# Performance work log

Measured on AMD Instinct MI355X. Metric: run time of the kernel, lower is better.

The kernel has to match this reference:

```python
import jax, jax.numpy as jnp
import numpy as np

B, T, D, H, O = 64, 1000, 16, 1024, 8
DT, TAU, G, PROB_CONN = 0.1, 1.0, 1.5, 0.25


def setup_inputs() -> dict:
    key = jax.random.key(0)
    k_in, k_h0, k_i2h, k_mask, k_val, k_h2o = jax.random.split(key, 6)
    inp = jax.random.normal(k_in, (B, T, D), dtype=jnp.float32)
    hidden = jax.random.normal(k_h0, (B, H), dtype=jnp.float32)
    # i2h: 1/sqrt(D) * randn(H, D)
    W_i2h = jax.random.normal(k_i2h, (H, D), dtype=jnp.float32) / np.sqrt(D)
    # h2h: sparse Gaussian, connection prob PROB_CONN, no self-connections,
    # std = g / sqrt(prob_conn * H)
    mask = (jax.random.uniform(k_mask, (H, H)) < PROB_CONN).astype(jnp.float32)
    mask = mask * (1.0 - jnp.eye(H, dtype=jnp.float32))
    sigma = G / np.sqrt(PROB_CONN * H)
    W_h2h = jax.random.normal(k_val, (H, H), dtype=jnp.float32) * sigma * mask
    # h2o: 1/sqrt(H) * randn(O, H)
    W_h2o = jax.random.normal(k_h2o, (O, H), dtype=jnp.float32) / np.sqrt(H)
    return {"input": inp, "hidden": hidden, "W_i2h": W_i2h, "W_h2h": W_h2h, "W_h2o": W_h2o}


def reference(input, hidden, W_i2h, W_h2h, W_h2o):
    a = DT / TAU  # leak factor
    # precompute input projection for all timesteps: [B,T,H]
    x_proj = jnp.einsum('btd,hd->bth', input, W_i2h)
    xs = jnp.swapaxes(x_proj, 0, 1)  # [T,B,H]

    def step(h, x_t):
        h = (1.0 - a) * h + a * (jnp.tanh(h) @ W_h2h.T + x_t)
        out = jnp.tanh(h) @ W_h2o.T
        return h, (out, h)

    _, (outs, hs) = jax.lax.scan(step, hidden, xs)
    outputs = jnp.swapaxes(outs, 0, 1)  # [B,T,O]
    hiddens = jnp.swapaxes(hs, 0, 1)    # [B,T,H]
    return outputs, hiddens
```

## Files before the change

### kernel.cpp

```cpp
#include <hip/hip_runtime.h>
#include <hip/hip_bf16.h>

#define BB 64
#define TT 1000
#define DD 16
#define HH 1024
#define OO 8

#define NGRP 16
#define GB   4
#define SJ   64
#define NJS  16
#define NBLK 256
#define NTH  512

__global__ __launch_bounds__(NTH, 2) void rnn_coop(
    const float* __restrict__ x,
    const float* __restrict__ h0,
    const float* __restrict__ Wi2h,
    const float* Wh2h,
    float* __restrict__ out_h,
    float* TH,
    unsigned* flags)
{
    __shared__ __align__(16) float THl[8][4][GB][36];
    __shared__ float SC[2][GB][SJ][9];
    __shared__ float XS[2][GB][20];

    const int tid = threadIdx.x;
    const int w   = tid >> 6;
    const int l   = tid & 63;
    const int bid = blockIdx.x;
    const int bg  = bid & (NGRP - 1);
    const int js  = bid >> 4;

    const int j16 = l & 15;
    const int k4  = l >> 4;
    const int jbase = js * SJ + j16 * 4;
    const int kbase = w * 128 + k4 * 32;

    float4 w4[4][8];
#pragma unroll
    for (int jj = 0; jj < 4; ++jj)
#pragma unroll
        for (int kq = 0; kq < 8; ++kq)
            w4[jj][kq] = *(const float4*)&Wh2h[(size_t)(jbase + jj) * HH + kbase + kq * 4];
#pragma unroll
    for (int jj = 0; jj < 4; ++jj)
#pragma unroll
        for (int kq = 0; kq < 8; ++kq)
            asm volatile("" : "+v"(w4[jj][kq].x), "+v"(w4[jj][kq].y),
                             "+v"(w4[jj][kq].z), "+v"(w4[jj][kq].w));

    const int fb = tid >> 6, fj = tid & 63;
    float h = 0.f;
    float wi[DD];
    if (tid < 256) {
        h = h0[(size_t)(bg * GB + fb) * HH + js * SJ + fj];
#pragma unroll
        for (int d = 0; d < DD; ++d) wi[d] = Wi2h[(js * SJ + fj) * DD + d];
        float th0 = tanhf(h);
        __hip_atomic_store(&TH[((size_t)(0 * NGRP + bg) * GB + fb) * HH + js * SJ + fj],
                           th0, __ATOMIC_RELAXED, __HIP_MEMORY_SCOPE_AGENT);
        asm volatile("s_waitcnt vmcnt(0)" ::: "memory");
        if (l == 0)
            __hip_atomic_store(&flags[((size_t)(0 * NGRP + bg) * NJS + js) * 16 + fb],
                               1u, __ATOMIC_RELAXED, __HIP_MEMORY_SCOPE_AGENT);
    }

    for (int t = 0; t < TT; ++t) {
        const int p = t & 1;

        {
            const unsigned target = (unsigned)(t + 1);
            const unsigned* fa = flags +
                ((size_t)(p * NGRP + bg) * NJS + (2 * w + (l >> 2))) * 16 + (l & 3);
            for (;;) {
                unsigned v = target;
                if (l < 8)
                    v = __hip_atomic_load(fa, __ATOMIC_RELAXED, __HIP_MEMORY_SCOPE_AGENT);
                if (__all((int)(v >= target))) break;
                __builtin_amdgcn_s_sleep(1);
            }
        }

        {
            const int sb = l >> 4, sq = l & 15;
            const float* base = TH + ((size_t)(p * NGRP + bg) * GB + sb) * HH + w * 128;
            const float* a0 = base + sq * 4;
            const float* a1 = base + (sq + 16) * 4;
            float4 v0, v1;
            asm volatile("global_load_dwordx4 %0, %2, off sc0 sc1\n\t"
                         "global_load_dwordx4 %1, %3, off sc0 sc1\n\t"
                         "s_waitcnt vmcnt(0)"
                         : "=&v"(v0), "=&v"(v1)
                         : "v"(a0), "v"(a1)
                         : "memory");
            int k40 = sq >> 3,        kk0 = (sq & 7) ^ k40;
            int k41 = (sq + 16) >> 3, kk1 = (sq & 7) ^ k41;
            *(float4*)&THl[w][k40][sb][kk0 * 4] = v0;
            *(float4*)&THl[w][k41][sb][kk1 * 4] = v1;
        }
        if (w == 0) {
            int sb = l >> 2, dq = (l & 3) * 4;
            if (l < 16) {
                float4 v = *(const float4*)&x[((size_t)(bg * GB + sb) * TT + t) * DD + dq];
                *(float4*)&XS[p][sb][dq] = v;
            }
        }
        asm volatile("s_waitcnt lgkmcnt(0)" ::: "memory");
        __builtin_amdgcn_sched_barrier(0);

        float acc[4][4];
#pragma unroll
        for (int jj = 0; jj < 4; ++jj)
#pragma unroll
            for (int m = 0; m < 4; ++m) acc[jj][m] = 0.f;
#pragma unroll
        for (int kq = 0; kq < 8; ++kq) {
            const int kks = (kq ^ k4) * 4;
#pragma unroll
            for (int m = 0; m < 4; ++m) {
                float4 tv = *(const float4*)&THl[w][k4][m][kks];
#pragma unroll
                for (int jj = 0; jj < 4; ++jj) {
                    acc[jj][m] += w4[jj][kq].x * tv.x;
                    acc[jj][m] += w4[jj][kq].y * tv.y;
                    acc[jj][m] += w4[jj][kq].z * tv.z;
                    acc[jj][m] += w4[jj][kq].w * tv.w;
                }
            }
        }

#pragma unroll
        for (int jj = 0; jj < 4; ++jj)
#pragma unroll
            for (int m = 0; m < 4; ++m) {
                float a = acc[jj][m];
                a += __shfl_xor(a, 16, 64);
                a += __shfl_xor(a, 32, 64);
                acc[jj][m] = a;
            }
        if (k4 == 0) {
#pragma unroll
            for (int m = 0; m < 4; ++m)
#pragma unroll
                for (int jj = 0; jj < 4; ++jj)
                    SC[p][m][j16 * 4 + jj][w] = acc[jj][m];
        }

        __syncthreads();

        if (tid < 256) {
            float z = 0.f;
#pragma unroll
            for (int ww = 0; ww < 8; ++ww) z += SC[p][fb][fj][ww];
            float xp = 0.f;
#pragma unroll
            for (int d = 0; d < DD; ++d) xp += wi[d] * XS[p][fb][d];
            h = 0.9f * h + 0.1f * (z + xp);
            float th = tanhf(h);
            __hip_atomic_store(
                &TH[((size_t)((p ^ 1) * NGRP + bg) * GB + fb) * HH + js * SJ + fj],
                th, __ATOMIC_RELAXED, __HIP_MEMORY_SCOPE_AGENT);
            asm volatile("s_waitcnt vmcnt(0)" ::: "memory");
            if (l == 0 && t + 1 < TT)
                __hip_atomic_store(
                    &flags[((size_t)((p ^ 1) * NGRP + bg) * NJS + js) * 16 + fb],
                    (unsigned)(t + 2), __ATOMIC_RELAXED, __HIP_MEMORY_SCOPE_AGENT);
            out_h[((size_t)(bg * GB + fb) * TT + t) * HH + js * SJ + fj] = h;
        }
    }
}

__global__ __launch_bounds__(256) void h2o_kernel(
    const float* __restrict__ hs,
    const float* __restrict__ Wh2o,
    float* __restrict__ out_o)
{
    __shared__ float Wl[OO * HH];
    for (int i = threadIdx.x; i < OO * HH; i += 256) Wl[i] = Wh2o[i];
    __syncthreads();

    const int w = threadIdx.x >> 6, l = threadIdx.x & 63;
    const size_t nrows = (size_t)BB * TT;
    for (size_t row = (size_t)blockIdx.x * 4 + w; row < nrows; row += (size_t)gridDim.x * 4) {
        const float* hr = hs + row * HH;
        float po[OO] = {0.f};
#pragma unroll
        for (int i = 0; i < 16; ++i) {
            int j = l + 64 * i;
            float th = tanhf(hr[j]);
#pragma unroll
            for (int o = 0; o < OO; ++o) po[o] += th * Wl[o * HH + j];
        }
#pragma unroll
        for (int s = 32; s; s >>= 1)
#pragma unroll
            for (int o = 0; o < OO; ++o) po[o] += __shfl_down(po[o], s, 64);
        if (l == 0) {
#pragma unroll
            for (int o = 0; o < OO; ++o) out_o[row * OO + o] = po[o];
        }
    }
}

__global__ __launch_bounds__(512) void rnn_fallback(
    const float* __restrict__ x, const float* __restrict__ h0,
    const float* __restrict__ Wi2h, const float* __restrict__ W,
    const float* __restrict__ Wh2o, float* __restrict__ out_o,
    float* __restrict__ out_h)
{
    const int b = blockIdx.x, t0 = threadIdx.x, j0 = 2 * t0;
    const int wave = t0 >> 6, lane = t0 & 63;
    __shared__ float th[HH];
    __shared__ float xs[DD];
    __shared__ float ored[8][OO];
    float wi[2][DD];
#pragma unroll
    for (int d = 0; d < DD; ++d) {
        wi[0][d] = Wi2h[j0 * DD + d];
        wi[1][d] = Wi2h[(j0 + 1) * DD + d];
    }
    float wo[2][OO];
#pragma unroll
    for (int o = 0; o < OO; ++o) {
        wo[0][o] = Wh2o[o * HH + j0];
        wo[1][o] = Wh2o[o * HH + j0 + 1];
    }
    float h[2] = { h0[b * HH + j0], h0[b * HH + j0 + 1] };
    th[j0] = tanhf(h[0]); th[j0 + 1] = tanhf(h[1]);
    if (t0 < DD) xs[t0] = x[(size_t)(b * TT) * DD + t0];
    __syncthreads();
    for (int t = 0; t < TT; ++t) {
        float a0 = 0.f, a1 = 0.f;
        const float* r0 = W + (size_t)j0 * HH;
        const float* r1 = W + (size_t)(j0 + 1) * HH;
#pragma unroll 4
        for (int k = 0; k < HH; k += 4) {
            float4 t4 = *(const float4*)&th[k];
            float4 wA = *(const float4*)(r0 + k);
            float4 wB = *(const float4*)(r1 + k);
            a0 += t4.x * wA.x + t4.y * wA.y + t4.z * wA.z + t4.w * wA.w;
            a1 += t4.x * wB.x + t4.y * wB.y + t4.z * wB.z + t4.w * wB.w;
        }
        float xp0 = 0.f, xp1 = 0.f;
#pragma unroll
        for (int d = 0; d < DD; ++d) { xp0 += xs[d] * wi[0][d]; xp1 += xs[d] * wi[1][d]; }
        h[0] = 0.9f * h[0] + 0.1f * (a0 + xp0);
        h[1] = 0.9f * h[1] + 0.1f * (a1 + xp1);
        float th0 = tanhf(h[0]), th1 = tanhf(h[1]);
        *(float2*)&out_h[((size_t)b * TT + t) * HH + j0] = make_float2(h[0], h[1]);
        float po[OO];
#pragma unroll
        for (int o = 0; o < OO; ++o) po[o] = th0 * wo[0][o] + th1 * wo[1][o];
#pragma unroll
        for (int s = 32; s; s >>= 1)
#pragma unroll
            for (int o = 0; o < OO; ++o) po[o] += __shfl_down(po[o], s, 64);
        __syncthreads();
        if (lane == 0)
#pragma unroll
            for (int o = 0; o < OO; ++o) ored[wave][o] = po[o];
        th[j0] = th0; th[j0 + 1] = th1;
        if (t0 < DD && t + 1 < TT) xs[t0] = x[(size_t)(b * TT + t + 1) * DD + t0];
        __syncthreads();
        if (t0 < OO) {
            float s = 0.f;
#pragma unroll
            for (int ww = 0; ww < 8; ++ww) s += ored[ww][t0];
            out_o[((size_t)b * TT + t) * OO + t0] = s;
        }
    }
}

extern "C" void kernel_launch(void* const* d_in, const int* in_sizes, int n_in,
                              void* d_out, int out_size, void* d_ws, size_t ws_size,
                              hipStream_t stream) {
    const float* x    = (const float*)d_in[0];
    const float* h0   = (const float*)d_in[1];
    const float* Wi2h = (const float*)d_in[2];
    const float* Wh2h = (const float*)d_in[3];
    const float* Wh2o = (const float*)d_in[4];

    float* out_o = (float*)d_out;
    float* out_h = out_o + (size_t)BB * TT * OO;

    const size_t th_bytes   = (size_t)2 * NGRP * GB * HH * sizeof(float);
    const size_t flag_bytes = (size_t)2 * NGRP * NJS * 16 * sizeof(unsigned);
    const size_t need       = th_bytes + flag_bytes;

    if (ws_size >= need) {
        float*    TH  = (float*)d_ws;
        unsigned* flg = (unsigned*)((char*)d_ws + th_bytes);
        hipMemsetAsync(flg, 0, flag_bytes, stream);
        rnn_coop<<<NBLK, NTH, 0, stream>>>(x, h0, Wi2h, Wh2h, out_h, TH, flg);
        h2o_kernel<<<2048, 256, 0, stream>>>(out_h, Wh2o, out_o);
    } else {
        rnn_fallback<<<BB, 512, 0, stream>>>(x, h0, Wi2h, Wh2h, Wh2o, out_o, out_h);
    }
}
```

Baseline: 5.409 ms.

## Pack timestep tag with tanh value to replace separate flag synchronization

Each tanh(h) value is stored as a 64-bit word holding both the value and the timestep tag. Consumers poll the data directly until every tag matches, so the per-step store-wait-then-flag handshake and the separate flag polling go away. This cuts one round trip of global-memory latency from the critical path of each of the 1000 sequential steps. The cost is double the bytes in the exchange buffer and re-reading the data on failed polls. The last step uses a one-shot flag to get around the ABA problem with the double buffer.

```diff
diff --git a/kernel.cpp b/kernel.cpp
--- a/kernel.cpp
+++ b/kernel.cpp
@@ -14,14 +14,187 @@
 #define NBLK 256
 #define NTH  512
 
-__global__ __launch_bounds__(NTH, 2) void rnn_coop(
+typedef unsigned long long u64;
+
+__global__ __launch_bounds__(NTH, 2) void rnn_coop_tag(
     const float* __restrict__ x,
     const float* __restrict__ h0,
     const float* __restrict__ Wi2h,
     const float* Wh2h,
     float* __restrict__ out_h,
-    float* TH,
+    u64* TH2,
     unsigned* flags)
+{
+    __shared__ __align__(16) float THl[8][4][GB][36];
+    __shared__ float SC[2][GB][SJ][9];
+    __shared__ float XS[2][GB][20];
+
+    const int tid = threadIdx.x;
+    const int w   = tid >> 6;
+    const int l   = tid & 63;
+    const int bid = blockIdx.x;
+    const int bg  = bid & (NGRP - 1);
+    const int js  = bid >> 4;
+
+    const int j16 = l & 15;
+    const int k4  = l >> 4;
+    const int jbase = js * SJ + j16 * 4;
+    const int kbase = w * 128 + k4 * 32;
+
+    float4 w4[4][8];
+#pragma unroll
+    for (int jj = 0; jj < 4; ++jj) {
+        const float* a = &Wh2h[(size_t)(jbase + jj) * HH + kbase];
+        asm volatile(
+            "global_load_dwordx4 %0, %8, off\n\t"
+            "global_load_dwordx4 %1, %8, off offset:16\n\t"
+            "global_load_dwordx4 %2, %8, off offset:32\n\t"
+            "global_load_dwordx4 %3, %8, off offset:48\n\t"
+            "global_load_dwordx4 %4, %8, off offset:64\n\t"
+            "global_load_dwordx4 %5, %8, off offset:80\n\t"
+            "global_load_dwordx4 %6, %8, off offset:96\n\t"
+            "global_load_dwordx4 %7, %8, off offset:112\n\t"
+            "s_waitcnt vmcnt(0)"
+            : "=&v"(w4[jj][0]), "=&v"(w4[jj][1]), "=&v"(w4[jj][2]), "=&v"(w4[jj][3]),
+              "=&v"(w4[jj][4]), "=&v"(w4[jj][5]), "=&v"(w4[jj][6]), "=&v"(w4[jj][7])
+            : "v"(a));
+    }
+
+    const int fb = tid >> 6, fj = tid & 63;
+    float h = 0.f;
+    float wi[DD];
+    if (tid < 256) {
+        h = h0[(size_t)(bg * GB + fb) * HH + js * SJ + fj];
+#pragma unroll
+        for (int d = 0; d < DD; ++d) wi[d] = Wi2h[(js * SJ + fj) * DD + d];
+        u64 pk = ((u64)1u << 32) | (u64)__float_as_uint(tanhf(h));
+        __hip_atomic_store(&TH2[((size_t)(0 * NGRP + bg) * GB + fb) * HH + js * SJ + fj],
+                           pk, __ATOMIC_RELAXED, __HIP_MEMORY_SCOPE_AGENT);
+    }
+
+    for (int t = 0; t < TT; ++t) {
+        const int p = t & 1;
+        const unsigned tg = (unsigned)(t + 1);
+        const int sb = l >> 4, sq = l & 15;
+
+        if (w == 0 && l < 16) {
+            int xb = l >> 2, dq = (l & 3) * 4;
+            float4 v = *(const float4*)&x[((size_t)(bg * GB + xb) * TT + t) * DD + dq];
+            *(float4*)&XS[p][xb][dq] = v;
+        }
+
+        const u64* base = TH2 + ((size_t)(p * NGRP + bg) * GB + sb) * HH
+                              + w * 128 + sq * 8;
+        uint4 A, B, C, D;
+        if (t == TT - 1) {
+            const unsigned* fa = flags +
+                ((size_t)bg * NJS + (2 * w + (l >> 2))) * 16 + (l & 3);
+            for (;;) {
+                unsigned v = 1u;
+                if (l < 8)
+                    v = __hip_atomic_load(fa, __ATOMIC_RELAXED, __HIP_MEMORY_SCOPE_AGENT);
+                if (__all((int)(v != 0))) break;
+                __builtin_amdgcn_s_sleep(1);
+            }
+        }
+        for (;;) {
+            asm volatile(
+                "global_load_dwordx4 %0, %4, off sc0 sc1\n\t"
+                "global_load_dwordx4 %1, %4, off offset:16 sc0 sc1\n\t"
+                "global_load_dwordx4 %2, %4, off offset:32 sc0 sc1\n\t"
+                "global_load_dwordx4 %3, %4, off offset:48 sc0 sc1\n\t"
+                "s_waitcnt vmcnt(0)"
+                : "=&v"(A), "=&v"(B), "=&v"(C), "=&v"(D)
+                : "v"(base) : "memory");
+            if (t == TT - 1) break;
+            unsigned bad = (A.y ^ tg) | (A.w ^ tg) | (B.y ^ tg) | (B.w ^ tg) |
+                           (C.y ^ tg) | (C.w ^ tg) | (D.y ^ tg) | (D.w ^ tg);
+            if (__all((int)(bad == 0))) break;
+            __builtin_amdgcn_s_sleep(1);
+        }
+
+        {
+            int Q0 = sq * 2, Q1 = sq * 2 + 1;
+            int k40 = Q0 >> 3, kk0 = (Q0 & 7) ^ k40;
+            int k41 = Q1 >> 3, kk1 = (Q1 & 7) ^ k41;
+            float4 f0 = make_float4(__uint_as_float(A.x), __uint_as_float(A.z),
+                                    __uint_as_float(B.x), __uint_as_float(B.z));
+            float4 f1 = make_float4(__uint_as_float(C.x), __uint_as_float(C.z),
+                                    __uint_as_float(D.x), __uint_as_float(D.z));
+            *(float4*)&THl[w][k40][sb][kk0 * 4] = f0;
+            *(float4*)&THl[w][k41][sb][kk1 * 4] = f1;
+        }
+        asm volatile("s_waitcnt lgkmcnt(0)" ::: "memory");
+        __builtin_amdgcn_sched_barrier(0);
+
+        float acc[4][4];
+#pragma unroll
+        for (int jj = 0; jj < 4; ++jj)
+#pragma unroll
+            for (int m = 0; m < 4; ++m) acc[jj][m] = 0.f;
+#pragma unroll
+        for (int kq = 0; kq < 8; ++kq) {
+            const int kks = (kq ^ k4) * 4;
+#pragma unroll
+            for (int m = 0; m < 4; ++m) {
+                float4 tv = *(const float4*)&THl[w][k4][m][kks];
+#pragma unroll
+                for (int jj = 0; jj < 4; ++jj) {
+                    acc[jj][m] += w4[jj][kq].x * tv.x;
+                    acc[jj][m] += w4[jj][kq].y * tv.y;
+                    acc[jj][m] += w4[jj][kq].z * tv.z;
+                    acc[jj][m] += w4[jj][kq].w * tv.w;
+                }
+            }
+        }
+
+#pragma unroll
+        for (int jj = 0; jj < 4; ++jj)
+#pragma unroll
+            for (int m = 0; m < 4; ++m) {
+                float a = acc[jj][m];
+                a += __shfl_xor(a, 16, 64);
+                a += __shfl_xor(a, 32, 64);
+                acc[jj][m] = a;
+            }
+        if (k4 == 0) {
+#pragma unroll
+            for (int m = 0; m < 4; ++m)
+#pragma unroll
+                for (int jj = 0; jj < 4; ++jj)
+                    SC[p][m][j16 * 4 + jj][w] = acc[jj][m];
+        }
+
+        __syncthreads();
+
+        if (tid < 256) {
+            float z = 0.f;
+#pragma unroll
+            for (int ww = 0; ww < 8; ++ww) z += SC[p][fb][fj][ww];
+            float xp = 0.f;
+#pragma unroll
+            for (int d = 0; d < DD; ++d) xp += wi[d] * XS[p][fb][d];
+            h = 0.9f * h + 0.1f * (z + xp);
+            float th = tanhf(h);
+            u64 pk = ((u64)(unsigned)(t + 2) << 32) | (u64)__float_as_uint(th);
+            __hip_atomic_store(
+                &TH2[((size_t)((p ^ 1) * NGRP + bg) * GB + fb) * HH + js * SJ + fj],
+                pk, __ATOMIC_RELAXED, __HIP_MEMORY_SCOPE_AGENT);
+            if (t == TT - 2) {
+                asm volatile("s_waitcnt vmcnt(0)" ::: "memory");
+                if (l == 0)
+                    __hip_atomic_store(&flags[((size_t)bg * NJS + js) * 16 + fb],
+                                       1u, __ATOMIC_RELAXED, __HIP_MEMORY_SCOPE_AGENT);
+            }
+            out_h[((size_t)(bg * GB + fb) * TT + t) * HH + js * SJ + fj] = h;
+        }
+    }
+}
+
+__global__ __launch_bounds__(NTH, 2) void rnn_coop_flag(
+    const float* __restrict__ x, const float* __restrict__ h0,
+    const float* __restrict__ Wi2h, const float* Wh2h,
+    float* __restrict__ out_h, float* TH, unsigned* flags)
 {
     __shared__ __align__(16) float THl[8][4][GB][36];
     __shared__ float SC[2][GB][SJ][9];
@@ -70,7 +243,6 @@
 
     for (int t = 0; t < TT; ++t) {
         const int p = t & 1;
-
         {
             const unsigned target = (unsigned)(t + 1);
             const unsigned* fa = flags +
@@ -83,7 +255,6 @@
                 __builtin_amdgcn_s_sleep(1);
             }
         }
-
         {
             const int sb = l >> 4, sq = l & 15;
             const float* base = TH + ((size_t)(p * NGRP + bg) * GB + sb) * HH + w * 128;
@@ -101,12 +272,10 @@
             *(float4*)&THl[w][k40][sb][kk0 * 4] = v0;
             *(float4*)&THl[w][k41][sb][kk1 * 4] = v1;
         }
-        if (w == 0) {
-            int sb = l >> 2, dq = (l & 3) * 4;
-            if (l < 16) {
-                float4 v = *(const float4*)&x[((size_t)(bg * GB + sb) * TT + t) * DD + dq];
-                *(float4*)&XS[p][sb][dq] = v;
-            }
+        if (w == 0 && l < 16) {
+            int sb2 = l >> 2, dq = (l & 3) * 4;
+            float4 v = *(const float4*)&x[((size_t)(bg * GB + sb2) * TT + t) * DD + dq];
+            *(float4*)&XS[p][sb2][dq] = v;
         }
         asm volatile("s_waitcnt lgkmcnt(0)" ::: "memory");
         __builtin_amdgcn_sched_barrier(0);
@@ -131,7 +300,6 @@
                 }
             }
         }
-
 #pragma unroll
         for (int jj = 0; jj < 4; ++jj)
 #pragma unroll
@@ -148,9 +316,7 @@
                 for (int jj = 0; jj < 4; ++jj)
                     SC[p][m][j16 * 4 + jj][w] = acc[jj][m];
         }
-
         __syncthreads();
-
         if (tid < 256) {
             float z = 0.f;
 #pragma unroll
@@ -174,8 +340,7 @@
 }
 
 __global__ __launch_bounds__(256) void h2o_kernel(
-    const float* __restrict__ hs,
-    const float* __restrict__ Wh2o,
+    const float* __restrict__ hs, const float* __restrict__ Wh2o,
     float* __restrict__ out_o)
 {
     __shared__ float Wl[OO * HH];
@@ -286,15 +451,22 @@
     float* out_o = (float*)d_out;
     float* out_h = out_o + (size_t)BB * TT * OO;
 
-    const size_t th_bytes   = (size_t)2 * NGRP * GB * HH * sizeof(float);
-    const size_t flag_bytes = (size_t)2 * NGRP * NJS * 16 * sizeof(unsigned);
-    const size_t need       = th_bytes + flag_bytes;
-
-    if (ws_size >= need) {
+    const size_t th2_bytes  = (size_t)2 * NGRP * GB * HH * sizeof(u64);
+    const size_t flg2_bytes = (size_t)NGRP * NJS * 16 * sizeof(unsigned);
+    const size_t th5_bytes  = (size_t)2 * NGRP * GB * HH * sizeof(float);
+    const size_t flg5_bytes = (size_t)2 * NGRP * NJS * 16 * sizeof(unsigned);
+
+    if (ws_size >= th2_bytes + flg2_bytes) {
+        u64*      TH2 = (u64*)d_ws;
+        unsigned* flg = (unsigned*)((char*)d_ws + th2_bytes);
+        hipMemsetAsync(flg, 0, flg2_bytes, stream);
+        rnn_coop_tag<<<NBLK, NTH, 0, stream>>>(x, h0, Wi2h, Wh2h, out_h, TH2, flg);
+        h2o_kernel<<<2048, 256, 0, stream>>>(out_h, Wh2o, out_o);
+    } else if (ws_size >= th5_bytes + flg5_bytes) {
         float*    TH  = (float*)d_ws;
-        unsigned* flg = (unsigned*)((char*)d_ws + th_bytes);
-        hipMemsetAsync(flg, 0, flag_bytes, stream);
-        rnn_coop<<<NBLK, NTH, 0, stream>>>(x, h0, Wi2h, Wh2h, out_h, TH, flg);
+        unsigned* flg = (unsigned*)((char*)d_ws + th5_bytes);
+        hipMemsetAsync(flg, 0, flg5_bytes, stream);
+        rnn_coop_flag<<<NBLK, NTH, 0, stream>>>(x, h0, Wi2h, Wh2h, out_h, TH, flg);
         h2o_kernel<<<2048, 256, 0, stream>>>(out_h, Wh2o, out_o);
     } else {
         rnn_fallback<<<BB, 512, 0, stream>>>(x, h0, Wi2h, Wh2h, Wh2o, out_o, out_h);
```

After: 6.382 ms. +18.0%, slower.
